# Kernel tuning notes

Hardware: AMD Instinct MI355X
Metric: run time of the kernel (lower is better)

Reference implementation:

```python
import jax, jax.numpy as jnp
import numpy as np

B, N, G, H, W = 4, 2000, 100, 1024, 1024
T = 200
POS_RATIO = 0.33
P_POS = int(T * POS_RATIO)  # 66, matches int(TRAIN_ROIS_PER_IMAGE * ROI_POSITIVE_RATIO)
P_NEG = T - P_POS           # 134 slots reserved for negatives
MASK_H, MASK_W = 28, 28
BBOX_STD = jnp.array([0.1, 0.1, 0.2, 0.2], jnp.float32)


def setup_inputs() -> dict:
    key = jax.random.key(0)
    ks = jax.random.split(key, 7)
    # GT boxes: (y1,x1) in [0,0.6], height/width in [0.05,0.35] -> valid, non-degenerate
    yx = jax.random.uniform(ks[0], (B, G, 2), minval=0.0, maxval=0.6)
    hw = jax.random.uniform(ks[1], (B, G, 2), minval=0.05, maxval=0.35)
    gt_boxes = jnp.concatenate([yx, yx + hw], axis=-1)
    gt_class_ids = jax.random.randint(ks[2], (B, G), 1, 81).astype(jnp.int32)
    gt_masks = jax.random.uniform(ks[3], (B, H, W, G)) < 0.5
    # Proposals: half are jittered copies of GT boxes (guarantees IoU>=0.5 positives),
    # half random boxes (negatives).
    reps = (N // 2) // G  # 10
    jit = jax.random.uniform(ks[4], (B, G * reps, 4), minval=-0.02, maxval=0.02)
    jittered = jnp.tile(gt_boxes, (1, reps, 1)) + jit
    pyx = jax.random.uniform(ks[5], (B, N - G * reps, 2), minval=0.0, maxval=0.6)
    phw = jax.random.uniform(ks[6], (B, N - G * reps, 2), minval=0.05, maxval=0.35)
    randprops = jnp.concatenate([pyx, pyx + phw], axis=-1)
    proposals = jnp.clip(jnp.concatenate([jittered, randprops], axis=1), 0.0, 1.0)
    return {"proposals": proposals, "gt_class_ids": gt_class_ids,
            "gt_boxes": gt_boxes, "gt_masks": gt_masks}


def _iou(b1, b2):
    # b1 [N,4], b2 [G,4] -> [N,G]  (pairwise IoU, same math as overlaps_graph)
    y1 = jnp.maximum(b1[:, None, 0], b2[None, :, 0])
    x1 = jnp.maximum(b1[:, None, 1], b2[None, :, 1])
    y2 = jnp.minimum(b1[:, None, 2], b2[None, :, 2])
    x2 = jnp.minimum(b1[:, None, 3], b2[None, :, 3])
    inter = jnp.maximum(x2 - x1, 0.0) * jnp.maximum(y2 - y1, 0.0)
    a1 = (b1[:, 2] - b1[:, 0]) * (b1[:, 3] - b1[:, 1])
    a2 = (b2[:, 2] - b2[:, 0]) * (b2[:, 3] - b2[:, 1])
    return inter / (a1[:, None] + a2[None, :] - inter)


def _refine(box, gt):
    # box_refinement_graph: [P,4] each -> [P,4] (dy,dx,log dh,log dw)
    h = box[:, 2] - box[:, 0]
    w = box[:, 3] - box[:, 1]
    cy = box[:, 0] + 0.5 * h
    cx = box[:, 1] + 0.5 * w
    gh = gt[:, 2] - gt[:, 0]
    gw = gt[:, 3] - gt[:, 1]
    gcy = gt[:, 0] + 0.5 * gh
    gcx = gt[:, 1] + 0.5 * gw
    return jnp.stack([(gcy - cy) / h, (gcx - cx) / w,
                      jnp.log(gh / h), jnp.log(gw / w)], axis=1)


def _crop_resize(masks_t, g, box):
    # tf.image.crop_and_resize for one ROI: masks_t [G,H,W] bool, g scalar idx, box [4]
    img = masks_t[g]  # [H,W] bool
    Hh, Ww = img.shape
    y1, x1, y2, x2 = box[0], box[1], box[2], box[3]
    ys = y1 * (Hh - 1) + jnp.arange(MASK_H, dtype=jnp.float32) * ((y2 - y1) * (Hh - 1) / (MASK_H - 1))
    xs = x1 * (Ww - 1) + jnp.arange(MASK_W, dtype=jnp.float32) * ((x2 - x1) * (Ww - 1) / (MASK_W - 1))
    y0f, x0f = jnp.floor(ys), jnp.floor(xs)
    y0 = jnp.clip(y0f, 0, Hh - 1).astype(jnp.int32)
    yb = jnp.clip(y0f + 1, 0, Hh - 1).astype(jnp.int32)
    x0 = jnp.clip(x0f, 0, Ww - 1).astype(jnp.int32)
    xb = jnp.clip(x0f + 1, 0, Ww - 1).astype(jnp.int32)
    fy = (ys - y0f)[:, None]
    fx = (xs - x0f)[None, :]
    v00 = img[y0[:, None], x0[None, :]].astype(jnp.float32)
    v01 = img[y0[:, None], xb[None, :]].astype(jnp.float32)
    v10 = img[yb[:, None], x0[None, :]].astype(jnp.float32)
    v11 = img[yb[:, None], xb[None, :]].astype(jnp.float32)
    top = v00 * (1.0 - fx) + v01 * fx
    bot = v10 * (1.0 - fx) + v11 * fx
    return top * (1.0 - fy) + bot * fy  # [28,28]


def _per_image(props, gt_ids, gt_bx, gt_mk, key):
    ov = _iou(props, gt_bx)                                   # [N,G]
    crowd = gt_ids < 0
    nc = gt_ids > 0
    ov_nc = jnp.where(nc[None, :], ov, -1.0)
    roi_iou_max = ov_nc.max(axis=1)
    crowd_iou_max = jnp.where(crowd[None, :], ov, -1.0).max(axis=1)
    no_crowd = crowd_iou_max < 1e-3
    pos_b = roi_iou_max >= 0.5
    neg_b = (roi_iou_max < 0.5) & no_crowd
    k1, k2 = jax.random.split(key)
    n = props.shape[0]
    # random_shuffle-then-take-k == top_k of uniform random scores over eligible rois
    pos_sc = jnp.where(pos_b, jax.random.uniform(k1, (n,)), -1.0)
    _, pos_idx = jax.lax.top_k(pos_sc, P_POS)
    n_pos = jnp.minimum(pos_b.sum(), P_POS)
    pos_valid = jnp.arange(P_POS) < n_pos
    # negative_count = int(pos_count / ratio) - pos_count, capped by slots/availability
    n_neg_tgt = (n_pos.astype(jnp.float32) / POS_RATIO).astype(jnp.int32) - n_pos
    neg_sc = jnp.where(neg_b, jax.random.uniform(k2, (n,)), -1.0)
    _, neg_idx = jax.lax.top_k(neg_sc, P_NEG)
    n_neg = jnp.minimum(jnp.minimum(neg_b.sum(), n_neg_tgt), P_NEG)
    neg_valid = jnp.arange(P_NEG) < n_neg
    pos_rois = props[pos_idx]                                 # [P_POS,4]
    assign = jnp.argmax(ov_nc[pos_idx], axis=1)               # gt assignment per positive roi
    roi_gt = gt_bx[assign]
    ids = jnp.where(pos_valid, gt_ids[assign], 0)
    deltas = jnp.where(pos_valid[:, None], _refine(pos_rois, roi_gt) / BBOX_STD, 0.0)
    masks_t = jnp.transpose(gt_mk, (2, 0, 1))                 # [G,H,W]
    masks = jax.vmap(lambda g, b: _crop_resize(masks_t, g, b))(assign, pos_rois)
    masks = jnp.where(pos_valid[:, None, None], jnp.round(masks), 0.0)
    rois = jnp.concatenate([jnp.where(pos_valid[:, None], pos_rois, 0.0),
                            jnp.where(neg_valid[:, None], props[neg_idx], 0.0)], axis=0)
    ids_full = jnp.concatenate([ids, jnp.zeros((P_NEG,), ids.dtype)])
    deltas_full = jnp.concatenate([deltas, jnp.zeros((P_NEG, 4), deltas.dtype)])
    masks_full = jnp.concatenate([masks, jnp.zeros((P_NEG, MASK_H, MASK_W), masks.dtype)])
    return rois, ids_full, deltas_full, masks_full


def reference(proposals, gt_class_ids, gt_boxes, gt_masks):
    keys = jax.random.split(jax.random.key(42), proposals.shape[0])
    return jax.vmap(_per_image)(proposals, gt_class_ids, gt_boxes, gt_masks, keys)
```

## Files before the change

kernel.cpp:

```cpp
#include <hip/hip_runtime.h>
#include <stdint.h>

#pragma clang fp contract(off)

#define BB 4
#define NN 2000
#define GG 100
#define HIMG 1024
#define WIMG 1024
#define PPOS 66
#define PNEG 134
#define TT 200
#define MH 28
#define MW 28
#define CHUNK 250
#define GRID 512
#define MAGIC 0x5EC7ED42

#define OFF_ROIS 0
#define OFF_IDS  (BB*TT*4)
#define OFF_DELT (BB*TT*4 + BB*TT)
#define OFF_MASK (BB*TT*4 + BB*TT + BB*TT*4)

#define WS_SCP(b)  ((b)*2048)
#define WS_SCN(b)  (8192 + (b)*2048)
#define WS_CNT     16384
#define WS_PIDX(b) (16512 + (b)*128)
#define WS_ASG(b)  (18048 + (b)*128)
#define WS_SFLG    18560
#define WS_DFLG    18600

#define SH_SC0    0
#define SH_SC1    8000
#define SH_MLIST  16000
#define SH_CNT    24000
#define SH_BASE   25024
#define SH_FILL   26048
#define SH_GT     27072
#define SH_GID    28672
#define SH_SPOS   29072
#define SH_SNEG   29336
#define SH_TOT    29872
#define SH_BYTES  29952
#define SHC_IY0   0
#define SHC_IY1   112
#define SHC_IX0   224
#define SHC_IX1   336
#define SHC_FY    448
#define SHC_FX    560
#define SHC_BOX   672

__device__ __forceinline__ void tf2x32(uint32_t k0, uint32_t k1, uint32_t& x0, uint32_t& x1){
  uint32_t ks2 = k0 ^ k1 ^ 0x1BD11BDAu;
  x0 += k0; x1 += k1;
#define TFR(r) { x0 += x1; x1 = (x1 << r) | (x1 >> (32 - r)); x1 ^= x0; }
  TFR(13) TFR(15) TFR(26) TFR(6)
  x0 += k1;  x1 += ks2 + 1u;
  TFR(17) TFR(29) TFR(16) TFR(24)
  x0 += ks2; x1 += k0 + 2u;
  TFR(13) TFR(15) TFR(26) TFR(6)
  x0 += k0;  x1 += k1 + 3u;
  TFR(17) TFR(29) TFR(16) TFR(24)
  x0 += k1;  x1 += ks2 + 4u;
  TFR(13) TFR(15) TFR(26) TFR(6)
  x0 += ks2; x1 += k0 + 5u;
#undef TFR
}

__device__ __forceinline__ float u01(uint32_t b){
  return __uint_as_float((b >> 9) | 0x3f800000u) - 1.0f;
}

__device__ __forceinline__ void img_keys(int b, uint32_t& k1a, uint32_t& k1b,
                                         uint32_t& k2a, uint32_t& k2b){
  uint32_t ia = 0u, ib = (uint32_t)b;
  tf2x32(0u, 42u, ia, ib);
  uint32_t a0 = 0u, c0 = 0u; tf2x32(ia, ib, a0, c0);
  uint32_t a1 = 0u, c1 = 1u; tf2x32(ia, ib, a1, c1);
  k1a = a0; k1b = c0; k2a = a1; k2b = c1;
}

__device__ __forceinline__ float iou2(float py1, float px1, float py2, float px2,
                                      float gy1, float gx1, float gy2, float gx2){
  float y1 = fmaxf(py1, gy1);
  float x1 = fmaxf(px1, gx1);
  float y2 = fminf(py2, gy2);
  float x2 = fminf(px2, gx2);
  float inter = fmaxf(x2 - x1, 0.0f) * fmaxf(y2 - y1, 0.0f);
  float a1 = (py2 - py1) * (px2 - px1);
  float a2 = (gy2 - gy1) * (gx2 - gx1);
  return inter / (a1 + a2 - inter);
}

__global__ __launch_bounds__(256, 2) void dtl_all(
    const float* __restrict__ props, const int* __restrict__ gids,
    const float* __restrict__ gboxes, const unsigned char* __restrict__ gmask,
    float* __restrict__ out, float* __restrict__ wsF, int* __restrict__ wsI)
{
  __shared__ __align__(16) unsigned char shB[SH_BYTES];
  const int blk = blockIdx.x;
  const int t = threadIdx.x;
  const int lane = t & 63, wave = t >> 6;

  float4* sGt  = (float4*)(shB + SH_GT);
  int*    sGid = (int*)(shB + SH_GID);

  if (blk < 32){
    const int cx = blk & 7, b = blk >> 3;
    if (t < GG){
      sGt[t]  = ((const float4*)(gboxes + b*GG*4))[t];
      sGid[t] = gids[b*GG + t];
    }
    __syncthreads();
    const int i = cx*CHUNK + t;
    if (t < CHUNK && i < NN){
      const float4 p = ((const float4*)(props + b*NN*4))[i];
      float best = -1.0f, cbest = -1.0f;
      for (int g = 0; g < GG; ++g){
        float4 gb = sGt[g];
        float v = iou2(p.x, p.y, p.z, p.w, gb.x, gb.y, gb.z, gb.w);
        int id = sGid[g];
        if (id > 0) best = fmaxf(best, v);
        else if (id < 0) cbest = fmaxf(cbest, v);
      }
      bool noc  = cbest < 1e-3f;
      bool posb = best >= 0.5f;
      bool negb = (best < 0.5f) && noc;
      uint32_t k1a, k1b, k2a, k2b;
      img_keys(b, k1a, k1b, k2a, k2b);
      uint32_t a = 0u, c = (uint32_t)i;
      tf2x32(k1a, k1b, a, c);
      uint32_t a2 = 0u, c2 = (uint32_t)i;
      tf2x32(k2a, k2b, a2, c2);
      wsF[WS_SCP(b) + i] = posb ? u01(a ^ c)   : -1.0f;
      wsF[WS_SCN(b) + i] = negb ? u01(a2 ^ c2) : -1.0f;
    }
    __syncthreads();
    if (t == 0){
      __threadfence();
      __hip_atomic_store(&wsI[WS_SFLG + blk], MAGIC, __ATOMIC_RELEASE,
                         __HIP_MEMORY_SCOPE_AGENT);
    }
  }

  if (blk < BB){
    const int b = blk;
    float* sSc0  = (float*)(shB + SH_SC0);
    float* sSc1  = (float*)(shB + SH_SC1);
    int*   mlist = (int*)(shB + SH_MLIST);
    int*   cnt   = (int*)(shB + SH_CNT);
    int*   base_ = (int*)(shB + SH_BASE);
    int*   fill  = (int*)(shB + SH_FILL);
    int*   slotPos = (int*)(shB + SH_SPOS);
    int*   slotNeg = (int*)(shB + SH_SNEG);
    int*   sTot  = (int*)(shB + SH_TOT);

    if (t < 8){
      while (__hip_atomic_load(&wsI[WS_SFLG + b*8 + t], __ATOMIC_ACQUIRE,
                               __HIP_MEMORY_SCOPE_AGENT) != MAGIC)
        __builtin_amdgcn_s_sleep(2);
    }
    __syncthreads();

    if (t < GG){
      sGt[t]  = ((const float4*)(gboxes + b*GG*4))[t];
      sGid[t] = gids[b*GG + t];
    }
    for (int j = t; j < NN/4; j += 256){
      ((float4*)sSc0)[j] = ((const float4*)(wsF + WS_SCP(b)))[j];
      ((float4*)sSc1)[j] = ((const float4*)(wsF + WS_SCN(b)))[j];
    }

    for (int a = 0; a < 2; ++a){
      const int cap = a ? PNEG : PPOS;
      const float* sc = a ? sSc1 : sSc0;
      cnt[t] = 0; fill[t] = 0;
      __syncthreads();
      for (int i = t; i < NN; i += 256){
        float v = sc[i];
        if (v >= 0.0f){
          int k = min((int)(v*256.0f), 255);
          atomicAdd(&cnt[k], 1);
        }
      }
      __syncthreads();
      if (wave == 0){
        int c0 = cnt[lane*4+0], c1 = cnt[lane*4+1], c2 = cnt[lane*4+2], c3 = cnt[lane*4+3];
        int p0 = c0, p1 = p0+c1, p2 = p1+c2, p3 = p2+c3;
        int inc = p3;
        for (int off = 1; off < 64; off <<= 1){
          int v = __shfl_up(inc, off);
          if (lane >= off) inc += v;
        }
        int excl = inc - p3;
        base_[lane*4+0] = excl;
        base_[lane*4+1] = excl + p0;
        base_[lane*4+2] = excl + p1;
        base_[lane*4+3] = excl + p2;
        if (lane == 63) sTot[a] = inc;
      }
      __syncthreads();
      for (int i = t; i < NN; i += 256){
        float v = sc[i];
        if (v >= 0.0f){
          int k = min((int)(v*256.0f), 255);
          int pos = base_[k] + atomicAdd(&fill[k], 1);
          mlist[pos] = i;
        }
      }
      __syncthreads();
      const int tot = sTot[a];
      int* slotArr = a ? slotNeg : slotPos;
      for (int i = t; i < NN; i += 256){
        float v = sc[i];
        if (v >= 0.0f){
          int k = min((int)(v*256.0f), 255);
          int S = tot - base_[k] - cnt[k];
          if (S < cap){
            int wr = 0;
            const int s0 = base_[k], e0 = s0 + cnt[k];
            for (int m = s0; m < e0; ++m){
              int j = mlist[m];
              float vj = sc[j];
              wr += (int)((vj > v) | ((vj == v) & (j < i)));
            }
            int slot = S + wr;
            if (slot < cap) slotArr[slot] = i;
          }
        }
      }
      __syncthreads();
    }

    const int npos = min(sTot[0], PPOS);
    int tgt = (int)((float)npos / 0.33f) - npos;
    if (tgt < 0) tgt = 0;
    const int nneg = min(min(sTot[1], tgt), PNEG);
    if (t == 0) wsI[WS_CNT + b*4] = npos;

    const float* pb = props + b*NN*4;
    if (t < TT){
      float r0=0,r1=0,r2=0,r3=0, idv=0, d0=0,d1=0,d2=0,d3=0;
      if (t < PPOS){
        if (t < npos){
          int idx = slotPos[t];
          float4 p = ((const float4*)pb)[idx];
          float bestv = -2.0f; int bg = 0;
          for (int g = 0; g < GG; ++g){
            float4 gb = sGt[g];
            float v = (sGid[g] > 0) ? iou2(p.x,p.y,p.z,p.w, gb.x,gb.y,gb.z,gb.w) : -1.0f;
            if (v > bestv){ bestv = v; bg = g; }
          }
          float4 gt = sGt[bg];
          float h  = p.z - p.x,        w  = p.w - p.y;
          float cy = p.x + 0.5f*h,     cx = p.y + 0.5f*w;
          float gh = gt.z - gt.x,      gw = gt.w - gt.y;
          float gcy = gt.x + 0.5f*gh,  gcx = gt.y + 0.5f*gw;
          r0 = p.x; r1 = p.y; r2 = p.z; r3 = p.w;
          idv = (float)sGid[bg];
          d0 = ((gcy - cy) / h) / 0.1f;
          d1 = ((gcx - cx) / w) / 0.1f;
          d2 = logf(gh / h) / 0.2f;
          d3 = logf(gw / w) / 0.2f;
          wsI[WS_PIDX(b) + t] = idx;
          wsI[WS_ASG(b) + t]  = bg;
        }
      } else {
        int pn = t - PPOS;
        if (pn < nneg){
          int idx = slotNeg[pn];
          float4 p = ((const float4*)pb)[idx];
          r0 = p.x; r1 = p.y; r2 = p.z; r3 = p.w;
        }
      }
      float* ro = out + OFF_ROIS + (b*TT + t)*4;
      ro[0] = r0; ro[1] = r1; ro[2] = r2; ro[3] = r3;
      out[OFF_IDS + b*TT + t] = idv;
      float* de = out + OFF_DELT + (b*TT + t)*4;
      de[0] = d0; de[1] = d1; de[2] = d2; de[3] = d3;
    }
    __syncthreads();
    if (t == 0){
      __threadfence();
      __hip_atomic_store(&wsI[WS_DFLG + b], MAGIC, __ATOMIC_RELEASE,
                         __HIP_MEMORY_SCOPE_AGENT);
    }
  }

  for (int s = blk; s < BB*TT; s += GRID){
    const int b = s / TT;
    const int p = s % TT;
    if (t == 0){
      while (__hip_atomic_load(&wsI[WS_DFLG + b], __ATOMIC_ACQUIRE,
                               __HIP_MEMORY_SCOPE_AGENT) != MAGIC)
        __builtin_amdgcn_s_sleep(2);
    }
    __syncthreads();
    const int npos = wsI[WS_CNT + b*4];
    float* mo = out + OFF_MASK + (size_t)s * (MH*MW);
    if (p >= npos){
      for (int pix = t; pix < MH*MW; pix += 256) mo[pix] = 0.0f;
      continue;
    }
    int*   iy0 = (int*)(shB + SHC_IY0);
    int*   iy1 = (int*)(shB + SHC_IY1);
    int*   ix0 = (int*)(shB + SHC_IX0);
    int*   ix1 = (int*)(shB + SHC_IX1);
    float* fy  = (float*)(shB + SHC_FY);
    float* fx  = (float*)(shB + SHC_FX);
    float* sbox= (float*)(shB + SHC_BOX);
    if (t == 0){
      int idx = wsI[WS_PIDX(b) + p];
      sbox[0] = props[(b*NN + idx)*4 + 0];
      sbox[1] = props[(b*NN + idx)*4 + 1];
      sbox[2] = props[(b*NN + idx)*4 + 2];
      sbox[3] = props[(b*NN + idx)*4 + 3];
    }
    __syncthreads();
    if (t < MH){
      float y1 = sbox[0], y2 = sbox[2];
      float stepy = (y2 - y1) * 1023.0f / 27.0f;
      float ys = y1 * 1023.0f + (float)t * stepy;
      float y0f = floorf(ys);
      iy0[t] = (int)fminf(fmaxf(y0f, 0.0f), 1023.0f);
      iy1[t] = (int)fminf(fmaxf(y0f + 1.0f, 0.0f), 1023.0f);
      fy[t] = ys - y0f;
      float x1 = sbox[1], x2 = sbox[3];
      float stepx = (x2 - x1) * 1023.0f / 27.0f;
      float xs = x1 * 1023.0f + (float)t * stepx;
      float x0f = floorf(xs);
      ix0[t] = (int)fminf(fmaxf(x0f, 0.0f), 1023.0f);
      ix1[t] = (int)fminf(fmaxf(x0f + 1.0f, 0.0f), 1023.0f);
      fx[t] = xs - x0f;
    }
    __syncthreads();
    const int g = wsI[WS_ASG(b) + p];
    const unsigned char* mb = gmask + (size_t)b * HIMG * WIMG * GG + g;
    for (int pix = t; pix < MH*MW; pix += 256){
      int r = pix / MW, c = pix - r*MW;
      size_t ro0 = (size_t)iy0[r] * WIMG;
      size_t ro1 = (size_t)iy1[r] * WIMG;
      float v00 = mb[(ro0 + (size_t)ix0[c]) * GG] ? 1.0f : 0.0f;
      float v01 = mb[(ro0 + (size_t)ix1[c]) * GG] ? 1.0f : 0.0f;
      float v10 = mb[(ro1 + (size_t)ix0[c]) * GG] ? 1.0f : 0.0f;
      float v11 = mb[(ro1 + (size_t)ix1[c]) * GG] ? 1.0f : 0.0f;
      float fxx = fx[c], fyy = fy[r];
      float top = v00 * (1.0f - fxx) + v01 * fxx;
      float bot = v10 * (1.0f - fxx) + v11 * fxx;
      float val = top * (1.0f - fyy) + bot * fyy;
      mo[pix] = rintf(val);
    }
    __syncthreads();
  }
}

extern "C" void kernel_launch(void* const* d_in, const int* in_sizes, int n_in,
                              void* d_out, int out_size, void* d_ws, size_t ws_size,
                              hipStream_t stream){
  const float* props  = (const float*)d_in[0];
  const int*   gids   = (const int*)d_in[1];
  const float* gboxes = (const float*)d_in[2];
  const unsigned char* gmask = (const unsigned char*)d_in[3];
  float* out = (float*)d_out;
  float* wsF = (float*)d_ws;
  int*   wsI = (int*)d_ws;

  dtl_all<<<GRID, 256, 0, stream>>>(props, gids, gboxes, gmask, out, wsF, wsI);
}
```

Before: 64.05 us.

## Split pos/neg selection across blocks, widen IoU chunks, skip waits for negative mask slots

The IoU/score stage now uses 16 chunks per image instead of 8, so 64 blocks share the work. Positive and negative bucket selection now run concurrently in separate blocks rather than back to back in one block, and mlist insertion is limited to buckets that can reach the cap. Mask blocks zero-fill negative slots without waiting on the selection flag and walk the slots in reverse order, so blocks free of dependencies start first. This shortens the serial critical path but adds more flag spin-waits across blocks.

Measured after the change: 52.32 us. 18.3% less time.

```diff
diff --git a/kernel.cpp b/kernel.cpp
--- a/kernel.cpp
+++ b/kernel.cpp
@@ -13,7 +13,9 @@
 #define TT 200
 #define MH 28
 #define MW 28
-#define CHUNK 250
+#define NCHUNK 16
+#define CHUNK 125
+#define ABLK (BB*NCHUNK)
 #define GRID 512
 #define MAGIC 0x5EC7ED42
 
@@ -28,10 +30,9 @@
 #define WS_PIDX(b) (16512 + (b)*128)
 #define WS_ASG(b)  (18048 + (b)*128)
 #define WS_SFLG    18560
-#define WS_DFLG    18600
+#define WS_DFLG    18624
 
 #define SH_SC0    0
-#define SH_SC1    8000
 #define SH_MLIST  16000
 #define SH_CNT    24000
 #define SH_BASE   25024
@@ -92,6 +93,71 @@
   return inter / (a1 + a2 - inter);
 }
 
+__device__ __forceinline__ int bucket_select(
+    const float* sc, int cap, int* slotArr,
+    int* cnt, int* base_, int* fill, int* mlist, int* sTot,
+    int t, int lane, int wave)
+{
+  cnt[t] = 0; fill[t] = 0;
+  __syncthreads();
+  for (int i = t; i < NN; i += 256){
+    float v = sc[i];
+    if (v >= 0.0f){
+      int k = min((int)(v*256.0f), 255);
+      atomicAdd(&cnt[k], 1);
+    }
+  }
+  __syncthreads();
+  if (wave == 0){
+    int c0 = cnt[lane*4+0], c1 = cnt[lane*4+1], c2 = cnt[lane*4+2], c3 = cnt[lane*4+3];
+    int p0 = c0, p1 = p0+c1, p2 = p1+c2, p3 = p2+c3;
+    int inc = p3;
+    for (int off = 1; off < 64; off <<= 1){
+      int v = __shfl_up(inc, off);
+      if (lane >= off) inc += v;
+    }
+    int excl = inc - p3;
+    base_[lane*4+0] = excl;
+    base_[lane*4+1] = excl + p0;
+    base_[lane*4+2] = excl + p1;
+    base_[lane*4+3] = excl + p2;
+    if (lane == 63) sTot[0] = inc;
+  }
+  __syncthreads();
+  const int tot = sTot[0];
+  for (int i = t; i < NN; i += 256){
+    float v = sc[i];
+    if (v >= 0.0f){
+      int k = min((int)(v*256.0f), 255);
+      if (tot - base_[k] - cnt[k] < cap){
+        int pos = base_[k] + atomicAdd(&fill[k], 1);
+        mlist[pos] = i;
+      }
+    }
+  }
+  __syncthreads();
+  for (int i = t; i < NN; i += 256){
+    float v = sc[i];
+    if (v >= 0.0f){
+      int k = min((int)(v*256.0f), 255);
+      int S = tot - base_[k] - cnt[k];
+      if (S < cap){
+        int wr = 0;
+        const int s0 = base_[k], e0 = s0 + cnt[k];
+        for (int m = s0; m < e0; ++m){
+          int j = mlist[m];
+          float vj = sc[j];
+          wr += (int)((vj > v) | ((vj == v) & (j < i)));
+        }
+        int slot = S + wr;
+        if (slot < cap) slotArr[slot] = i;
+      }
+    }
+  }
+  __syncthreads();
+  return tot;
+}
+
 __global__ __launch_bounds__(256, 2) void dtl_all(
     const float* __restrict__ props, const int* __restrict__ gids,
     const float* __restrict__ gboxes, const unsigned char* __restrict__ gmask,
@@ -104,16 +170,24 @@
 
   float4* sGt  = (float4*)(shB + SH_GT);
   int*    sGid = (int*)(shB + SH_GID);
-
-  if (blk < 32){
-    const int cx = blk & 7, b = blk >> 3;
+  float*  sSc  = (float*)(shB + SH_SC0);
+  int*    mlist= (int*)(shB + SH_MLIST);
+  int*    cnt  = (int*)(shB + SH_CNT);
+  int*    base_= (int*)(shB + SH_BASE);
+  int*    fill = (int*)(shB + SH_FILL);
+  int*    slotPos = (int*)(shB + SH_SPOS);
+  int*    slotNeg = (int*)(shB + SH_SNEG);
+  int*    sTot = (int*)(shB + SH_TOT);
+
+  if (blk < ABLK){
+    const int cx = blk & (NCHUNK-1), b = blk >> 4;
     if (t < GG){
       sGt[t]  = ((const float4*)(gboxes + b*GG*4))[t];
       sGid[t] = gids[b*GG + t];
     }
     __syncthreads();
     const int i = cx*CHUNK + t;
-    if (t < CHUNK && i < NN){
+    if (t < CHUNK){
       const float4 p = ((const float4*)(props + b*NN*4))[i];
       float best = -1.0f, cbest = -1.0f;
       for (int g = 0; g < GG; ++g){
@@ -145,103 +219,29 @@
 
   if (blk < BB){
     const int b = blk;
-    float* sSc0  = (float*)(shB + SH_SC0);
-    float* sSc1  = (float*)(shB + SH_SC1);
-    int*   mlist = (int*)(shB + SH_MLIST);
-    int*   cnt   = (int*)(shB + SH_CNT);
-    int*   base_ = (int*)(shB + SH_BASE);
-    int*   fill  = (int*)(shB + SH_FILL);
-    int*   slotPos = (int*)(shB + SH_SPOS);
-    int*   slotNeg = (int*)(shB + SH_SNEG);
-    int*   sTot  = (int*)(shB + SH_TOT);
-
-    if (t < 8){
-      while (__hip_atomic_load(&wsI[WS_SFLG + b*8 + t], __ATOMIC_ACQUIRE,
+    if (t < NCHUNK){
+      while (__hip_atomic_load(&wsI[WS_SFLG + b*NCHUNK + t], __ATOMIC_ACQUIRE,
                                __HIP_MEMORY_SCOPE_AGENT) != MAGIC)
         __builtin_amdgcn_s_sleep(2);
     }
     __syncthreads();
-
     if (t < GG){
       sGt[t]  = ((const float4*)(gboxes + b*GG*4))[t];
       sGid[t] = gids[b*GG + t];
     }
-    for (int j = t; j < NN/4; j += 256){
-      ((float4*)sSc0)[j] = ((const float4*)(wsF + WS_SCP(b)))[j];
-      ((float4*)sSc1)[j] = ((const float4*)(wsF + WS_SCN(b)))[j];
-    }
-
-    for (int a = 0; a < 2; ++a){
-      const int cap = a ? PNEG : PPOS;
-      const float* sc = a ? sSc1 : sSc0;
-      cnt[t] = 0; fill[t] = 0;
-      __syncthreads();
-      for (int i = t; i < NN; i += 256){
-        float v = sc[i];
-        if (v >= 0.0f){
-          int k = min((int)(v*256.0f), 255);
-          atomicAdd(&cnt[k], 1);
-        }
-      }
-      __syncthreads();
-      if (wave == 0){
-        int c0 = cnt[lane*4+0], c1 = cnt[lane*4+1], c2 = cnt[lane*4+2], c3 = cnt[lane*4+3];
-        int p0 = c0, p1 = p0+c1, p2 = p1+c2, p3 = p2+c3;
-        int inc = p3;
-        for (int off = 1; off < 64; off <<= 1){
-          int v = __shfl_up(inc, off);
-          if (lane >= off) inc += v;
-        }
-        int excl = inc - p3;
-        base_[lane*4+0] = excl;
-        base_[lane*4+1] = excl + p0;
-        base_[lane*4+2] = excl + p1;
-        base_[lane*4+3] = excl + p2;
-        if (lane == 63) sTot[a] = inc;
-      }
-      __syncthreads();
-      for (int i = t; i < NN; i += 256){
-        float v = sc[i];
-        if (v >= 0.0f){
-          int k = min((int)(v*256.0f), 255);
-          int pos = base_[k] + atomicAdd(&fill[k], 1);
-          mlist[pos] = i;
-        }
-      }
-      __syncthreads();
-      const int tot = sTot[a];
-      int* slotArr = a ? slotNeg : slotPos;
-      for (int i = t; i < NN; i += 256){
-        float v = sc[i];
-        if (v >= 0.0f){
-          int k = min((int)(v*256.0f), 255);
-          int S = tot - base_[k] - cnt[k];
-          if (S < cap){
-            int wr = 0;
-            const int s0 = base_[k], e0 = s0 + cnt[k];
-            for (int m = s0; m < e0; ++m){
-              int j = mlist[m];
-              float vj = sc[j];
-              wr += (int)((vj > v) | ((vj == v) & (j < i)));
-            }
-            int slot = S + wr;
-            if (slot < cap) slotArr[slot] = i;
-          }
-        }
-      }
-      __syncthreads();
-    }
-
-    const int npos = min(sTot[0], PPOS);
-    int tgt = (int)((float)npos / 0.33f) - npos;
-    if (tgt < 0) tgt = 0;
-    const int nneg = min(min(sTot[1], tgt), PNEG);
+    for (int j = t; j < NN/4; j += 256)
+      ((float4*)sSc)[j] = ((const float4*)(wsF + WS_SCP(b)))[j];
+
+    int tot = bucket_select(sSc, PPOS, slotPos, cnt, base_, fill, mlist, sTot,
+                            t, lane, wave);
+    const int npos = min(tot, PPOS);
     if (t == 0) wsI[WS_CNT + b*4] = npos;
 
     const float* pb = props + b*NN*4;
     if (t < TT){
-      float r0=0,r1=0,r2=0,r3=0, idv=0, d0=0,d1=0,d2=0,d3=0;
+      float idv = 0, d0=0, d1=0, d2=0, d3=0;
       if (t < PPOS){
+        float r0=0, r1=0, r2=0, r3=0;
         if (t < npos){
           int idx = slotPos[t];
           float4 p = ((const float4*)pb)[idx];
@@ -265,16 +265,9 @@
           wsI[WS_PIDX(b) + t] = idx;
           wsI[WS_ASG(b) + t]  = bg;
         }
-      } else {
-        int pn = t - PPOS;
-        if (pn < nneg){
-          int idx = slotNeg[pn];
-          float4 p = ((const float4*)pb)[idx];
-          r0 = p.x; r1 = p.y; r2 = p.z; r3 = p.w;
-        }
+        float* ro = out + OFF_ROIS + (b*TT + t)*4;
+        ro[0] = r0; ro[1] = r1; ro[2] = r2; ro[3] = r3;
       }
-      float* ro = out + OFF_ROIS + (b*TT + t)*4;
-      ro[0] = r0; ro[1] = r1; ro[2] = r2; ro[3] = r3;
       out[OFF_IDS + b*TT + t] = idv;
       float* de = out + OFF_DELT + (b*TT + t)*4;
       de[0] = d0; de[1] = d1; de[2] = d2; de[3] = d3;
@@ -287,9 +280,19 @@
     }
   }
 
-  for (int s = blk; s < BB*TT; s += GRID){
-    const int b = s / TT;
-    const int p = s % TT;
+  if (blk >= BB && blk < 2*BB){
+    const int b = blk - BB;
+    if (t < NCHUNK){
+      while (__hip_atomic_load(&wsI[WS_SFLG + b*NCHUNK + t], __ATOMIC_ACQUIRE,
+                               __HIP_MEMORY_SCOPE_AGENT) != MAGIC)
+        __builtin_amdgcn_s_sleep(2);
+    }
+    __syncthreads();
+    for (int j = t; j < NN/4; j += 256)
+      ((float4*)sSc)[j] = ((const float4*)(wsF + WS_SCN(b)))[j];
+
+    int tot1 = bucket_select(sSc, PNEG, slotNeg, cnt, base_, fill, mlist, sTot,
+                             t, lane, wave);
     if (t == 0){
       while (__hip_atomic_load(&wsI[WS_DFLG + b], __ATOMIC_ACQUIRE,
                                __HIP_MEMORY_SCOPE_AGENT) != MAGIC)
@@ -297,7 +300,36 @@
     }
     __syncthreads();
     const int npos = wsI[WS_CNT + b*4];
+    int tgt = (int)((float)npos / 0.33f) - npos;
+    if (tgt < 0) tgt = 0;
+    const int nneg = min(min(tot1, tgt), PNEG);
+    if (t < PNEG){
+      float r0=0, r1=0, r2=0, r3=0;
+      if (t < nneg){
+        int idx = slotNeg[t];
+        float4 p = ((const float4*)(props + b*NN*4))[idx];
+        r0 = p.x; r1 = p.y; r2 = p.z; r3 = p.w;
+      }
+      float* ro = out + OFF_ROIS + (b*TT + PPOS + t)*4;
+      ro[0] = r0; ro[1] = r1; ro[2] = r2; ro[3] = r3;
+    }
+  }
+
+  for (int s = (BB*TT - 1) - blk; s >= 0; s -= GRID){
+    const int b = s / TT;
+    const int p = s % TT;
     float* mo = out + OFF_MASK + (size_t)s * (MH*MW);
+    if (p >= PPOS){
+      for (int pix = t; pix < MH*MW; pix += 256) mo[pix] = 0.0f;
+      continue;
+    }
+    if (t == 0){
+      while (__hip_atomic_load(&wsI[WS_DFLG + b], __ATOMIC_ACQUIRE,
+                               __HIP_MEMORY_SCOPE_AGENT) != MAGIC)
+        __builtin_amdgcn_s_sleep(2);
+    }
+    __syncthreads();
+    const int npos = wsI[WS_CNT + b*4];
     if (p >= npos){
       for (int pix = t; pix < MH*MW; pix += 256) mo[pix] = 0.0f;
       continue;
```
